# Performance work log

Measured on AMD Instinct MI355X. Metric: run time of the kernel, lower is better.

The kernel has to match this reference:

```python
import jax, jax.numpy as jnp
import numpy as np

FP8_MAX = 448.0  # finfo(float8_e4m3fn).max
EPS = 1e-12


def fp8_quantize_rowwise(x, scale_ub=None):
    """Per-row fp8 e4m3 quantization (fbgemm quantize_fp8_per_row semantics).
    Returns (q_fp8 [rows, K], recip_scale [rows, 1] fp32).
    """
    amax = jnp.max(jnp.abs(x), axis=-1, keepdims=True)  # [rows,1]
    if scale_ub is not None:
        amax = jnp.clip(amax, EPS, scale_ub)
    else:
        amax = jnp.maximum(amax, EPS)
    scale = FP8_MAX / amax  # [rows,1]
    q = jnp.clip(x * scale, -FP8_MAX, FP8_MAX).astype(jnp.float8_e4m3fn)
    return q, (1.0 / scale).astype(jnp.float32)


def setup_inputs() -> dict:
    key = jax.random.key(0)
    k1, k2, k3 = jax.random.split(key, 3)
    M, K, N = 8192, 4096, 4096
    input = jax.random.normal(k1, (M, K), dtype=jnp.float32)
    weight = jax.random.normal(k2, (N, K), dtype=jnp.float32) * 0.02
    bias = jax.random.normal(k3, (N,), dtype=jnp.float32)
    return {"input": input, "weight": weight, "bias": bias}


def reference(input, weight, bias):
    # Weight quantization (done once at load time in the torch module)
    qweight, w_scale = fp8_quantize_rowwise(weight)          # [N,K], [N,1]
    # Runtime per-row quantization of the activation
    qinput, x_scale = fp8_quantize_rowwise(input)            # [M,K], [M,1]
    # Scaled fp8 GEMM: dequantize via row-wise scales on output
    acc = jnp.matmul(qinput.astype(jnp.float32),
                     qweight.astype(jnp.float32).T)          # [M,N]
    out = acc * x_scale * w_scale.T + bias[None, :]
    return out.astype(jnp.float32)
```

## Files before the change

kernel.cpp:

```cpp
#include <hip/hip_runtime.h>
#include <cstdint>
#include <cstddef>

typedef float f32x16 __attribute__((ext_vector_type(16)));
typedef int i32x4 __attribute__((ext_vector_type(4)));
typedef int i32x8 __attribute__((ext_vector_type(8)));

#define FP8_MAX 448.0f

#define GL(gp, lp)                                               \
  __builtin_amdgcn_global_load_lds(                              \
      (const __attribute__((address_space(1))) void*)(gp),       \
      (__attribute__((address_space(3))) void*)(lp), 16, 0, 0)

__device__ __forceinline__ uint32_t pack4_e4m3(float a, float b, float c, float d) {
  int p = __builtin_amdgcn_cvt_pk_fp8_f32(a, b, 0, false);
  p = __builtin_amdgcn_cvt_pk_fp8_f32(c, d, p, true);
  return (uint32_t)p;
}

__global__ __launch_bounds__(256) void quant_rowwise(
    const float* __restrict__ X, const float* __restrict__ W,
    uint8_t* __restrict__ QA, uint8_t* __restrict__ QW,
    float* __restrict__ xsc, float* __restrict__ wsc, int K, int M) {
  const int row = blockIdx.x;
  const float* src;
  uint8_t* q;
  float* rec;
  if (row < M) {
    src = X + (size_t)row * K; q = QA + (size_t)row * K; rec = xsc + row;
  } else {
    const int r = row - M;
    src = W + (size_t)r * K; q = QW + (size_t)r * K; rec = wsc + r;
  }
  const int tid = threadIdx.x;
  const float4* __restrict__ x4 = (const float4*)src;
  float4 v[4];
  float am = 0.0f;
#pragma unroll
  for (int i = 0; i < 4; ++i) {
    v[i] = x4[i * 256 + tid];
    am = fmaxf(am, fmaxf(fmaxf(fabsf(v[i].x), fabsf(v[i].y)),
                         fmaxf(fabsf(v[i].z), fabsf(v[i].w))));
  }
#pragma unroll
  for (int off = 32; off > 0; off >>= 1)
    am = fmaxf(am, __shfl_xor(am, off));
  __shared__ float smax[4];
  const int wave = tid >> 6, lane = tid & 63;
  if (lane == 0) smax[wave] = am;
  __syncthreads();
  am = fmaxf(fmaxf(smax[0], smax[1]), fmaxf(smax[2], smax[3]));
  am = fmaxf(am, 1e-12f);
  const float scale = FP8_MAX / am;
  if (tid == 0) rec[0] = 1.0f / scale;
  uint32_t* __restrict__ q32 = (uint32_t*)q;
#pragma unroll
  for (int i = 0; i < 4; ++i) {
    float a = fminf(fmaxf(v[i].x * scale, -FP8_MAX), FP8_MAX);
    float b = fminf(fmaxf(v[i].y * scale, -FP8_MAX), FP8_MAX);
    float c = fminf(fmaxf(v[i].z * scale, -FP8_MAX), FP8_MAX);
    float d = fminf(fmaxf(v[i].w * scale, -FP8_MAX), FP8_MAX);
    q32[i * 256 + tid] = pack4_e4m3(a, b, c, d);
  }
}


#define MMS(TM, TN, A, B)                                          \
  acc[TM][TN] = __builtin_amdgcn_mfma_scale_f32_32x32x64_f8f6f4(   \
      (A), (B), acc[TM][TN], 0, 0, 0, 0x7F7F7F7F, 0, 0x7F7F7F7F);

#define STAGE(h, kt, bi)                                                    \
  do {                                                                      \
    const uint8_t* sp = ((h) < 2 ? Aq + aoff : Bq + boff) +                 \
                        (size_t)((h) & 1) * 128 * K + (size_t)(kt) * 64;    \
    GL(sp, &lds[(bi) * 32768 + ((h) < 2 ? 0 : 16384) + ((h) & 1) * 8192 +  \
                w * 1024]);                                                 \
  } while (0)

__device__ __forceinline__ i32x8 ldfrag(const uint8_t* p, int off) {
  i32x4 lo = *(const i32x4*)(p + off);
  i32x4 hi = *(const i32x4*)(p + (off ^ 16));
  return __builtin_shufflevector(lo, hi, 0, 1, 2, 3, 4, 5, 6, 7);
}

__global__ __launch_bounds__(512, 1) void gemm_fp8(
    const uint8_t* __restrict__ Aq, const uint8_t* __restrict__ Bq,
    const float* __restrict__ xs, const float* __restrict__ wsc,
    const float* __restrict__ bias, float* __restrict__ C,
    int M, int N, int K) {
  __shared__ __align__(16) uint8_t lds[98304];
  const int tid = threadIdx.x;
  const int w = tid >> 6, lane = tid & 63;
  const int wrow = w >> 2, wcol = w & 3;

  int bid = (int)blockIdx.x;
  bid = (bid & 7) * 64 + (bid >> 3);
  const int bm = bid & 31, bn = bid >> 5;
  const int row0 = bm * 256, col0 = bn * 256;

  const int srow = lane >> 2;
  const int scol = 16 * ((lane & 3) ^ ((lane >> 3) & 3));
  const size_t aoff = (size_t)(row0 + 16 * w + srow) * K + scol;
  const size_t boff = (size_t)(col0 + 16 * w + srow) * K + scol;

  const int ln31 = lane & 31;
  const int g2 = (lane >> 5) * 2;
  const int h = (ln31 >> 1) & 3;
  const int o0 = 16 * (g2 ^ h);
  const int arow = (wrow * 128 + ln31) * 64 + o0;
  const int brow = (wcol * 64 + ln31) * 64 + o0;

  f32x16 zero = {};
  f32x16 acc[4][2];
#pragma unroll
  for (int m = 0; m < 4; ++m)
#pragma unroll
    for (int n = 0; n < 2; ++n) acc[m][n] = zero;

  const int nk = K / 64;

  STAGE(0, 0, 0); STAGE(1, 0, 0); STAGE(2, 0, 0); STAGE(3, 0, 0);
  STAGE(0, 1, 1); STAGE(1, 1, 1); STAGE(2, 1, 1); STAGE(3, 1, 1);

  for (int t = 0; t < nk; ++t) {
    const int bi = t % 3;
    const int pb = (t + 2) % 3;
    const int pf = (t + 2 < nk) ? t + 2 : t;
    const int bA = bi * 32768;
    const int bB = bA + 16384;

    asm volatile("s_waitcnt vmcnt(4)" ::: "memory");
    __builtin_amdgcn_s_barrier();

    i32x8 a0 = ldfrag(lds, bA + arow);
    i32x8 b0 = ldfrag(lds, bB + brow);
    i32x8 b1 = ldfrag(lds, bB + brow + 2048);
    i32x8 a1 = ldfrag(lds, bA + arow + 2048);
    i32x8 a2 = ldfrag(lds, bA + arow + 4096);
    i32x8 a3 = ldfrag(lds, bA + arow + 6144);

    STAGE(0, pf, pb); STAGE(1, pf, pb); STAGE(2, pf, pb); STAGE(3, pf, pb);

    __builtin_amdgcn_s_setprio(1);
    MMS(0, 0, a0, b0) MMS(0, 1, a0, b1)
    MMS(1, 0, a1, b0) MMS(1, 1, a1, b1)
    MMS(2, 0, a2, b0) MMS(2, 1, a2, b1)
    MMS(3, 0, a3, b0) MMS(3, 1, a3, b1)
    __builtin_amdgcn_s_setprio(0);
  }

  const int cl = lane & 31;
  const int rtop = (lane >> 5) * 4;
#pragma unroll
  for (int tm = 0; tm < 4; ++tm) {
#pragma unroll
    for (int tn = 0; tn < 2; ++tn) {
      const int col = col0 + wcol * 64 + tn * 32 + cl;
      const float wsn = wsc[col];
      const float bb = bias[col];
      const int rowb = row0 + wrow * 128 + tm * 32 + rtop;
#pragma unroll
      for (int q = 0; q < 4; ++q) {
        const float4 xq = *(const float4*)&xs[rowb + 8 * q];
        const float xa[4] = {xq.x, xq.y, xq.z, xq.w};
#pragma unroll
        for (int j = 0; j < 4; ++j) {
          const int r = rowb + 8 * q + j;
          C[(size_t)r * N + col] = fmaf(acc[tm][tn][4 * q + j] * xa[j], wsn, bb);
        }
      }
    }
  }
}

extern "C" void kernel_launch(void* const* d_in, const int* in_sizes, int n_in,
                              void* d_out, int out_size, void* d_ws, size_t ws_size,
                              hipStream_t stream) {
  const float* input = (const float*)d_in[0];
  const float* weight = (const float*)d_in[1];
  const float* bias = (const float*)d_in[2];
  float* out = (float*)d_out;

  const int K = 4096;
  const int N = in_sizes[2];
  const int M = in_sizes[0] / K;

  uint8_t* qA = (uint8_t*)d_ws;
  uint8_t* qW = qA + (size_t)M * K;
  float* xsc = (float*)(qW + (size_t)N * K);
  float* wsc = xsc + M;

  quant_rowwise<<<M + N, 256, 0, stream>>>(input, weight, qA, qW, xsc, wsc, K, M);

  dim3 grid((M / 256) * (N / 256));
  gemm_fp8<<<grid, 512, 0, stream>>>(qA, qW, xsc, wsc, bias, out, M, N, K);
}
```

Before: 191.7 us.

## Pre-tile quantized weights for direct register loads, bypass LDS for B operand

The weight quantizer now writes fp8 weights in a K-block-major tiled layout, so each GEMM lane can read its B fragment straight from global memory into registers. Only the A operand is still staged through LDS, which halves the LDS footprint and the LDS traffic. B fragments are double-buffered in registers one k-step ahead, with the loop unrolled by two and explicit waitcnt and sched barriers. The cost is more global loads per wave, reliance on L2 reuse for B, and a quantize kernel whose weight stores are strided rather than contiguous.

```diff
diff --git a/kernel.cpp b/kernel.cpp
--- a/kernel.cpp
+++ b/kernel.cpp
@@ -21,18 +21,14 @@
 
 __global__ __launch_bounds__(256) void quant_rowwise(
     const float* __restrict__ X, const float* __restrict__ W,
-    uint8_t* __restrict__ QA, uint8_t* __restrict__ QW,
-    float* __restrict__ xsc, float* __restrict__ wsc, int K, int M) {
+    uint8_t* __restrict__ QA, uint8_t* __restrict__ QWT,
+    float* __restrict__ xsc, float* __restrict__ wsc, int K, int M, int N) {
   const int row = blockIdx.x;
-  const float* src;
-  uint8_t* q;
-  float* rec;
-  if (row < M) {
-    src = X + (size_t)row * K; q = QA + (size_t)row * K; rec = xsc + row;
-  } else {
-    const int r = row - M;
-    src = W + (size_t)r * K; q = QW + (size_t)r * K; rec = wsc + r;
-  }
+  const bool is_w = row >= M;
+  const int r = is_w ? row - M : row;
+  const float* src = (is_w ? W : X) + (size_t)r * K;
+  float* rec = (is_w ? wsc : xsc) + r;
+
   const int tid = threadIdx.x;
   const float4* __restrict__ x4 = (const float4*)src;
   float4 v[4];
@@ -54,14 +50,20 @@
   am = fmaxf(am, 1e-12f);
   const float scale = FP8_MAX / am;
   if (tid == 0) rec[0] = 1.0f / scale;
-  uint32_t* __restrict__ q32 = (uint32_t*)q;
+
 #pragma unroll
   for (int i = 0; i < 4; ++i) {
     float a = fminf(fmaxf(v[i].x * scale, -FP8_MAX), FP8_MAX);
     float b = fminf(fmaxf(v[i].y * scale, -FP8_MAX), FP8_MAX);
     float c = fminf(fmaxf(v[i].z * scale, -FP8_MAX), FP8_MAX);
     float d = fminf(fmaxf(v[i].w * scale, -FP8_MAX), FP8_MAX);
-    q32[i * 256 + tid] = pack4_e4m3(a, b, c, d);
+    const uint32_t p = pack4_e4m3(a, b, c, d);
+    if (!is_w) {
+      ((uint32_t*)(QA + (size_t)r * K))[i * 256 + tid] = p;
+    } else {
+      ((uint32_t*)QWT)[(size_t)(i * 16 + (tid >> 4)) * (N * 16) +
+                       (size_t)r * 16 + (tid & 15)] = p;
+    }
   }
 }
 
@@ -70,12 +72,22 @@
   acc[TM][TN] = __builtin_amdgcn_mfma_scale_f32_32x32x64_f8f6f4(   \
       (A), (B), acc[TM][TN], 0, 0, 0, 0x7F7F7F7F, 0, 0x7F7F7F7F);
 
-#define STAGE(h, kt, bi)                                                    \
-  do {                                                                      \
-    const uint8_t* sp = ((h) < 2 ? Aq + aoff : Bq + boff) +                 \
-                        (size_t)((h) & 1) * 128 * K + (size_t)(kt) * 64;    \
-    GL(sp, &lds[(bi) * 32768 + ((h) < 2 ? 0 : 16384) + ((h) & 1) * 8192 +  \
-                w * 1024]);                                                 \
+#define STAGEA(KT, BI)                                                     \
+  do {                                                                     \
+    GL(Aq + aoff + (size_t)(KT) * 64, &lds[(BI) * 16384 + w * 2048]);      \
+    GL(Aq + aoff2 + (size_t)(KT) * 64,                                     \
+       &lds[(BI) * 16384 + w * 2048 + 1024]);                              \
+  } while (0)
+
+#define LOADB(B0, B1, TT)                                                  \
+  do {                                                                     \
+    const uint8_t* bp = BqT + (size_t)(TT) * nstride + bbase;              \
+    i32x4 l0 = *(const i32x4*)(bp);                                        \
+    i32x4 h0 = *(const i32x4*)(bp + 16);                                   \
+    i32x4 l1 = *(const i32x4*)(bp + 2048);                                 \
+    i32x4 h1 = *(const i32x4*)(bp + 2064);                                 \
+    B0 = __builtin_shufflevector(l0, h0, 0, 1, 2, 3, 4, 5, 6, 7);          \
+    B1 = __builtin_shufflevector(l1, h1, 0, 1, 2, 3, 4, 5, 6, 7);          \
   } while (0)
 
 __device__ __forceinline__ i32x8 ldfrag(const uint8_t* p, int off) {
@@ -84,12 +96,36 @@
   return __builtin_shufflevector(lo, hi, 0, 1, 2, 3, 4, 5, 6, 7);
 }
 
+#define ITER(BC0, BC1, BN0, BN1, T)                                        \
+  do {                                                                     \
+    __builtin_amdgcn_s_barrier();                                          \
+    __builtin_amdgcn_sched_barrier(0);                                     \
+    const int pf = ((T) + 2 < nk) ? (T) + 2 : (T);                         \
+    const int t1 = ((T) + 1 < nk) ? (T) + 1 : (T);                         \
+    STAGEA(pf, ((T) + 2) % 3);                                             \
+    LOADB(BN0, BN1, t1);                                                   \
+    const int cb = ((T) % 3) * 16384 + arow;                               \
+    i32x8 a0 = ldfrag(lds, cb);                                            \
+    i32x8 a1 = ldfrag(lds, cb + 2048);                                     \
+    i32x8 a2 = ldfrag(lds, cb + 4096);                                     \
+    i32x8 a3 = ldfrag(lds, cb + 6144);                                     \
+    __builtin_amdgcn_sched_barrier(0);                                     \
+    asm volatile("s_waitcnt vmcnt(6) lgkmcnt(0)" ::: "memory");            \
+    __builtin_amdgcn_sched_barrier(0);                                     \
+    __builtin_amdgcn_s_setprio(1);                                         \
+    MMS(0, 0, a0, BC0) MMS(0, 1, a0, BC1)                                  \
+    MMS(1, 0, a1, BC0) MMS(1, 1, a1, BC1)                                  \
+    MMS(2, 0, a2, BC0) MMS(2, 1, a2, BC1)                                  \
+    MMS(3, 0, a3, BC0) MMS(3, 1, a3, BC1)                                  \
+    __builtin_amdgcn_s_setprio(0);                                         \
+  } while (0)
+
 __global__ __launch_bounds__(512, 1) void gemm_fp8(
-    const uint8_t* __restrict__ Aq, const uint8_t* __restrict__ Bq,
+    const uint8_t* __restrict__ Aq, const uint8_t* __restrict__ BqT,
     const float* __restrict__ xs, const float* __restrict__ wsc,
     const float* __restrict__ bias, float* __restrict__ C,
     int M, int N, int K) {
-  __shared__ __align__(16) uint8_t lds[98304];
+  __shared__ __align__(16) uint8_t lds[49152];
   const int tid = threadIdx.x;
   const int w = tid >> 6, lane = tid & 63;
   const int wrow = w >> 2, wcol = w & 3;
@@ -99,17 +135,19 @@
   const int bm = bid & 31, bn = bid >> 5;
   const int row0 = bm * 256, col0 = bn * 256;
 
+  const int ln31 = lane & 31;
+  const size_t nstride = (size_t)N * 64;
+
   const int srow = lane >> 2;
   const int scol = 16 * ((lane & 3) ^ ((lane >> 3) & 3));
-  const size_t aoff = (size_t)(row0 + 16 * w + srow) * K + scol;
-  const size_t boff = (size_t)(col0 + 16 * w + srow) * K + scol;
-
-  const int ln31 = lane & 31;
+  const size_t aoff = (size_t)(row0 + w * 32 + srow) * K + scol;
+  const size_t aoff2 = aoff + (size_t)16 * K;
+
   const int g2 = (lane >> 5) * 2;
-  const int h = (ln31 >> 1) & 3;
-  const int o0 = 16 * (g2 ^ h);
+  const int o0 = 16 * (g2 ^ ((ln31 >> 1) & 3));
   const int arow = (wrow * 128 + ln31) * 64 + o0;
-  const int brow = (wcol * 64 + ln31) * 64 + o0;
+
+  const size_t bbase = (size_t)(col0 + wcol * 64 + ln31) * 64 + (lane >> 5) * 32;
 
   f32x16 zero = {};
   f32x16 acc[4][2];
@@ -119,35 +157,17 @@
     for (int n = 0; n < 2; ++n) acc[m][n] = zero;
 
   const int nk = K / 64;
-
-  STAGE(0, 0, 0); STAGE(1, 0, 0); STAGE(2, 0, 0); STAGE(3, 0, 0);
-  STAGE(0, 1, 1); STAGE(1, 1, 1); STAGE(2, 1, 1); STAGE(3, 1, 1);
-
-  for (int t = 0; t < nk; ++t) {
-    const int bi = t % 3;
-    const int pb = (t + 2) % 3;
-    const int pf = (t + 2 < nk) ? t + 2 : t;
-    const int bA = bi * 32768;
-    const int bB = bA + 16384;
-
-    asm volatile("s_waitcnt vmcnt(4)" ::: "memory");
-    __builtin_amdgcn_s_barrier();
-
-    i32x8 a0 = ldfrag(lds, bA + arow);
-    i32x8 b0 = ldfrag(lds, bB + brow);
-    i32x8 b1 = ldfrag(lds, bB + brow + 2048);
-    i32x8 a1 = ldfrag(lds, bA + arow + 2048);
-    i32x8 a2 = ldfrag(lds, bA + arow + 4096);
-    i32x8 a3 = ldfrag(lds, bA + arow + 6144);
-
-    STAGE(0, pf, pb); STAGE(1, pf, pb); STAGE(2, pf, pb); STAGE(3, pf, pb);
-
-    __builtin_amdgcn_s_setprio(1);
-    MMS(0, 0, a0, b0) MMS(0, 1, a0, b1)
-    MMS(1, 0, a1, b0) MMS(1, 1, a1, b1)
-    MMS(2, 0, a2, b0) MMS(2, 1, a2, b1)
-    MMS(3, 0, a3, b0) MMS(3, 1, a3, b1)
-    __builtin_amdgcn_s_setprio(0);
+  i32x8 bc0, bc1, bn0, bn1;
+
+  STAGEA(0, 0);
+  STAGEA(1, 1);
+  LOADB(bc0, bc1, 0);
+  __builtin_amdgcn_sched_barrier(0);
+  asm volatile("s_waitcnt vmcnt(6)" ::: "memory");
+
+  for (int t = 0; t < nk; t += 2) {
+    ITER(bc0, bc1, bn0, bn1, t);
+    ITER(bn0, bn1, bc0, bc1, t + 1);
   }
 
   const int cl = lane & 31;
@@ -187,12 +207,13 @@
   const int M = in_sizes[0] / K;
 
   uint8_t* qA = (uint8_t*)d_ws;
-  uint8_t* qW = qA + (size_t)M * K;
-  float* xsc = (float*)(qW + (size_t)N * K);
+  uint8_t* qWT = qA + (size_t)M * K;
+  float* xsc = (float*)(qWT + (size_t)N * K);
   float* wsc = xsc + M;
 
-  quant_rowwise<<<M + N, 256, 0, stream>>>(input, weight, qA, qW, xsc, wsc, K, M);
+  quant_rowwise<<<M + N, 256, 0, stream>>>(input, weight, qA, qWT, xsc, wsc,
+                                           K, M, N);
 
   dim3 grid((M / 256) * (N / 256));
-  gemm_fp8<<<grid, 512, 0, stream>>>(qA, qW, xsc, wsc, bias, out, M, N, K);
-}
+  gemm_fp8<<<grid, 512, 0, stream>>>(qA, qWT, xsc, wsc, bias, out, M, N, K);
+}
```

Result: slower. 213.6 us (+11.4%).

## Interleave LDS fragment loads, global prefetch and MFMAs in phased barrier schedule

Applied to the files above, without the earlier changes.

Splits each k-iteration of the fp8 GEMM into four phases. Each phase loads one A fragment, issues part of the next-stage global-to-LDS prefetch, and then runs two MFMAs between barriers and priority raises. The staging layout is reorganized so each wave loads 32 contiguous rows of A and B with two loads, with A and B in separate triple-buffered regions. The goal is to overlap LDS reads, global loads and matrix ops more finely, at the cost of many extra workgroup barriers per iteration. The quant kernel's branch is also rewritten as selects.

```diff
diff --git a/kernel.cpp b/kernel.cpp
--- a/kernel.cpp
+++ b/kernel.cpp
@@ -24,15 +24,12 @@
     uint8_t* __restrict__ QA, uint8_t* __restrict__ QW,
     float* __restrict__ xsc, float* __restrict__ wsc, int K, int M) {
   const int row = blockIdx.x;
-  const float* src;
-  uint8_t* q;
-  float* rec;
-  if (row < M) {
-    src = X + (size_t)row * K; q = QA + (size_t)row * K; rec = xsc + row;
-  } else {
-    const int r = row - M;
-    src = W + (size_t)r * K; q = QW + (size_t)r * K; rec = wsc + r;
-  }
+  const bool is_w = row >= M;
+  const int r = is_w ? row - M : row;
+  const float* src = (is_w ? W : X) + (size_t)r * K;
+  uint8_t* q = (is_w ? QW : QA) + (size_t)r * K;
+  float* rec = (is_w ? wsc : xsc) + r;
+
   const int tid = threadIdx.x;
   const float4* __restrict__ x4 = (const float4*)src;
   float4 v[4];
@@ -70,12 +67,19 @@
   acc[TM][TN] = __builtin_amdgcn_mfma_scale_f32_32x32x64_f8f6f4(   \
       (A), (B), acc[TM][TN], 0, 0, 0, 0x7F7F7F7F, 0, 0x7F7F7F7F);
 
-#define STAGE(h, kt, bi)                                                    \
-  do {                                                                      \
-    const uint8_t* sp = ((h) < 2 ? Aq + aoff : Bq + boff) +                 \
-                        (size_t)((h) & 1) * 128 * K + (size_t)(kt) * 64;    \
-    GL(sp, &lds[(bi) * 32768 + ((h) < 2 ? 0 : 16384) + ((h) & 1) * 8192 +  \
-                w * 1024]);                                                 \
+#define STAGEA(KT, BI)                                                     \
+  do {                                                                     \
+    GL(Aq + aoff + (size_t)(KT) * 64, &lds[(BI) * 16384 + w * 2048]);      \
+    GL(Aq + aoff2 + (size_t)(KT) * 64,                                     \
+       &lds[(BI) * 16384 + w * 2048 + 1024]);                              \
+  } while (0)
+
+#define STAGEB(KT, BI)                                                     \
+  do {                                                                     \
+    GL(Bq + boff + (size_t)(KT) * 64,                                      \
+       &lds[49152 + (BI) * 16384 + w * 2048]);                             \
+    GL(Bq + boff2 + (size_t)(KT) * 64,                                     \
+       &lds[49152 + (BI) * 16384 + w * 2048 + 1024]);                      \
   } while (0)
 
 __device__ __forceinline__ i32x8 ldfrag(const uint8_t* p, int off) {
@@ -99,15 +103,17 @@
   const int bm = bid & 31, bn = bid >> 5;
   const int row0 = bm * 256, col0 = bn * 256;
 
+  const int ln31 = lane & 31;
+
   const int srow = lane >> 2;
   const int scol = 16 * ((lane & 3) ^ ((lane >> 3) & 3));
-  const size_t aoff = (size_t)(row0 + 16 * w + srow) * K + scol;
-  const size_t boff = (size_t)(col0 + 16 * w + srow) * K + scol;
-
-  const int ln31 = lane & 31;
+  const size_t aoff = (size_t)(row0 + w * 32 + srow) * K + scol;
+  const size_t aoff2 = aoff + (size_t)16 * K;
+  const size_t boff = (size_t)(col0 + w * 32 + srow) * K + scol;
+  const size_t boff2 = boff + (size_t)16 * K;
+
   const int g2 = (lane >> 5) * 2;
-  const int h = (ln31 >> 1) & 3;
-  const int o0 = 16 * (g2 ^ h);
+  const int o0 = 16 * (g2 ^ ((ln31 >> 1) & 3));
   const int arow = (wrow * 128 + ln31) * 64 + o0;
   const int brow = (wcol * 64 + ln31) * 64 + o0;
 
@@ -120,34 +126,53 @@
 
   const int nk = K / 64;
 
-  STAGE(0, 0, 0); STAGE(1, 0, 0); STAGE(2, 0, 0); STAGE(3, 0, 0);
-  STAGE(0, 1, 1); STAGE(1, 1, 1); STAGE(2, 1, 1); STAGE(3, 1, 1);
+  STAGEA(0, 0); STAGEB(0, 0);
+  STAGEA(1, 1); STAGEB(1, 1);
+  asm volatile("s_waitcnt vmcnt(4)" ::: "memory");
+  __builtin_amdgcn_s_barrier();
 
   for (int t = 0; t < nk; ++t) {
-    const int bi = t % 3;
+    const int sA = (t % 3) * 16384;
+    const int sB = 49152 + (t % 3) * 16384;
     const int pb = (t + 2) % 3;
     const int pf = (t + 2 < nk) ? t + 2 : t;
-    const int bA = bi * 32768;
-    const int bB = bA + 16384;
-
+
+    i32x8 b0 = ldfrag(lds, sB + brow);
+    i32x8 b1 = ldfrag(lds, sB + brow + 2048);
+    i32x8 a0 = ldfrag(lds, sA + arow);
+    STAGEB(pf, pb);
+    __builtin_amdgcn_s_barrier();
+    asm volatile("s_waitcnt lgkmcnt(0)" ::: "memory");
+    __builtin_amdgcn_s_setprio(1);
+    MMS(0, 0, a0, b0) MMS(0, 1, a0, b1)
+    __builtin_amdgcn_s_setprio(0);
+    __builtin_amdgcn_s_barrier();
+
+    i32x8 a1 = ldfrag(lds, sA + arow + 2048);
+    STAGEA(pf, pb);
+    __builtin_amdgcn_s_barrier();
+    asm volatile("s_waitcnt lgkmcnt(0)" ::: "memory");
+    __builtin_amdgcn_s_setprio(1);
+    MMS(1, 0, a1, b0) MMS(1, 1, a1, b1)
+    __builtin_amdgcn_s_setprio(0);
+    __builtin_amdgcn_s_barrier();
+
+    i32x8 a2 = ldfrag(lds, sA + arow + 4096);
+    __builtin_amdgcn_s_barrier();
+    asm volatile("s_waitcnt lgkmcnt(0)" ::: "memory");
+    __builtin_amdgcn_s_setprio(1);
+    MMS(2, 0, a2, b0) MMS(2, 1, a2, b1)
+    __builtin_amdgcn_s_setprio(0);
+    __builtin_amdgcn_s_barrier();
+
+    i32x8 a3 = ldfrag(lds, sA + arow + 6144);
     asm volatile("s_waitcnt vmcnt(4)" ::: "memory");
     __builtin_amdgcn_s_barrier();
-
-    i32x8 a0 = ldfrag(lds, bA + arow);
-    i32x8 b0 = ldfrag(lds, bB + brow);
-    i32x8 b1 = ldfrag(lds, bB + brow + 2048);
-    i32x8 a1 = ldfrag(lds, bA + arow + 2048);
-    i32x8 a2 = ldfrag(lds, bA + arow + 4096);
-    i32x8 a3 = ldfrag(lds, bA + arow + 6144);
-
-    STAGE(0, pf, pb); STAGE(1, pf, pb); STAGE(2, pf, pb); STAGE(3, pf, pb);
-
-    __builtin_amdgcn_s_setprio(1);
-    MMS(0, 0, a0, b0) MMS(0, 1, a0, b1)
-    MMS(1, 0, a1, b0) MMS(1, 1, a1, b1)
-    MMS(2, 0, a2, b0) MMS(2, 1, a2, b1)
+    asm volatile("s_waitcnt lgkmcnt(0)" ::: "memory");
+    __builtin_amdgcn_s_setprio(1);
     MMS(3, 0, a3, b0) MMS(3, 1, a3, b1)
     __builtin_amdgcn_s_setprio(0);
+    __builtin_amdgcn_s_barrier();
   }
 
   const int cl = lane & 31;
```

Measured after the change: 195.6 us. +2.1%, slower.
